# Optimization experiments

Hardware: AMD Instinct MI355X
Metric: run time of the kernel (lower is better)

Reference implementation:

```python
import jax, jax.numpy as jnp
import numpy as np

B, NK, TK, H = 16, 2048, 4096, 256


def setup_inputs() -> dict:
    key = jax.random.key(0)
    ks = jax.random.split(key, 9)
    s = 0.02  # init scale for weights
    return {
        "s_t_hat": jax.random.normal(ks[0], (B, 2 * H), dtype=jnp.float32),
        "encoder_outputs_node": jax.random.normal(ks[1], (B, NK, H), dtype=jnp.float32),
        "node_to_token": jax.random.uniform(ks[2], (B, NK, TK), dtype=jnp.float32),
        "enc_padding_mask_node": jnp.ones((B, NK), dtype=jnp.float32),
        "graph": jax.random.uniform(ks[3], (B, NK, NK), dtype=jnp.float32),
        "flow": jax.random.uniform(ks[4], (B, NK), dtype=jnp.float32),
        "W_c_w": jax.random.normal(ks[5], (1, H), dtype=jnp.float32) * s,
        "enc_proj_w": jax.random.normal(ks[6], (H, H), dtype=jnp.float32) * s,
        "dec_proj_w": jax.random.normal(ks[7], (2 * H, H), dtype=jnp.float32) * s,
        "dec_proj_b": jnp.zeros((H,), dtype=jnp.float32),
        "v_node_w": jax.random.normal(ks[8], (H, 1), dtype=jnp.float32) * s,
    }


def reference(s_t_hat, encoder_outputs_node, node_to_token, enc_padding_mask_node,
              graph, flow, W_c_w, enc_proj_w, dec_proj_w, dec_proj_b, v_node_w):
    # additive attention scoring over graph nodes
    enc_feat = jnp.einsum('bkh,hd->bkd', encoder_outputs_node, enc_proj_w)   # (b,nk,h)
    dec_fea = s_t_hat @ dec_proj_w + dec_proj_b                              # (b,h)
    _flow_feature = flow[..., None] @ W_c_w  # computed in original but unused (dead code)
    e = jnp.tanh(enc_feat + dec_fea[:, None, :])                             # (b,nk,h)
    scores = jnp.squeeze(e @ v_node_w, -1)                                   # (b,nk)
    # masked softmax with renormalization
    attn_ = jax.nn.softmax(scores, axis=1) * enc_padding_mask_node
    attn = attn_ / jnp.sum(attn_, axis=1, keepdims=True)                     # (b,nk)
    # project node attention to token space, renormalize
    tok_ = jnp.einsum('bk,bkt->bt', attn, node_to_token)                     # (b,tk)
    tok = tok_ / jnp.sum(tok_, axis=1, keepdims=True)
    # context vector
    c_t = jnp.einsum('bk,bkh->bh', attn, encoder_outputs_node)               # (b,h)
    # multi-hop graph diffusion
    one_hop = jnp.einsum('bk,bkm->bm', attn, graph)                          # (b,nk)
    two_hop = jnp.einsum('bk,bkm->bm', one_hop, graph)                       # (b,nk)
    flow_out = attn * 0.33333 + one_hop * 0.33333 + two_hop * 0.33333        # (b,nk)
    return (c_t, attn, tok, flow_out)
```

## Files before the change

### kernel.cpp

```cpp
#include <hip/hip_runtime.h>
#include <cstddef>

#define BB 16
#define NK 2048
#define TK 4096
#define HH 256
#define H2 512

__global__ void k_dec_fea(const float* __restrict__ s_t_hat,
                          const float* __restrict__ Wd,
                          const float* __restrict__ bd,
                          float* __restrict__ dec_fea) {
    int b = blockIdx.x, ks = blockIdx.y;
    int d = threadIdx.x;
    __shared__ float s[64];
    if (d < 64) s[d] = s_t_hat[b * H2 + ks * 64 + d];
    __syncthreads();
    float acc = (ks == 0) ? bd[d] : 0.f;
    #pragma unroll
    for (int j = 0; j < 64; ++j)
        acc = fmaf(s[j], Wd[(ks * 64 + j) * HH + d], acc);
    atomicAdd(&dec_fea[b * HH + d], acc);
}

__global__ __launch_bounds__(256) void k_scores(const float* __restrict__ enc,
                         const float* __restrict__ Wenc,
                         const float* __restrict__ dec_fea,
                         const float* __restrict__ v,
                         float* __restrict__ scores) {
    int b   = blockIdx.y;
    int k0  = blockIdx.x * 32;
    int tid = threadIdx.x;
    int lane = tid & 63;
    int wv   = tid >> 6;

    __shared__ float4 encSV[32 * 64];
    const float4* baseV = (const float4*)(enc + ((size_t)b * NK + k0) * HH);
    #pragma unroll
    for (int r = 0; r < 8; ++r) encSV[r * 256 + tid] = baseV[r * 256 + tid];
    __syncthreads();

    const float4* Wv = (const float4*)Wenc;
    float4 acc[8];
    #pragma unroll
    for (int i = 0; i < 8; ++i) acc[i] = make_float4(0.f, 0.f, 0.f, 0.f);

    for (int h4 = 0; h4 < 64; ++h4) {
        float4 w0 = Wv[(h4 * 4 + 0) * 64 + lane];
        float4 w1 = Wv[(h4 * 4 + 1) * 64 + lane];
        float4 w2 = Wv[(h4 * 4 + 2) * 64 + lane];
        float4 w3 = Wv[(h4 * 4 + 3) * 64 + lane];
        #pragma unroll
        for (int i = 0; i < 8; ++i) {
            float4 e = encSV[(wv * 8 + i) * 64 + h4];
            acc[i].x = fmaf(e.x, w0.x, acc[i].x); acc[i].y = fmaf(e.x, w0.y, acc[i].y);
            acc[i].z = fmaf(e.x, w0.z, acc[i].z); acc[i].w = fmaf(e.x, w0.w, acc[i].w);
            acc[i].x = fmaf(e.y, w1.x, acc[i].x); acc[i].y = fmaf(e.y, w1.y, acc[i].y);
            acc[i].z = fmaf(e.y, w1.z, acc[i].z); acc[i].w = fmaf(e.y, w1.w, acc[i].w);
            acc[i].x = fmaf(e.z, w2.x, acc[i].x); acc[i].y = fmaf(e.z, w2.y, acc[i].y);
            acc[i].z = fmaf(e.z, w2.z, acc[i].z); acc[i].w = fmaf(e.z, w2.w, acc[i].w);
            acc[i].x = fmaf(e.w, w3.x, acc[i].x); acc[i].y = fmaf(e.w, w3.y, acc[i].y);
            acc[i].z = fmaf(e.w, w3.z, acc[i].z); acc[i].w = fmaf(e.w, w3.w, acc[i].w);
        }
    }

    float4 df = ((const float4*)(dec_fea + b * HH))[lane];
    float4 vv = ((const float4*)v)[lane];
    #pragma unroll
    for (int i = 0; i < 8; ++i) {
        float p = tanhf(acc[i].x + df.x) * vv.x
                + tanhf(acc[i].y + df.y) * vv.y
                + tanhf(acc[i].z + df.z) * vv.z
                + tanhf(acc[i].w + df.w) * vv.w;
        #pragma unroll
        for (int off = 32; off > 0; off >>= 1) p += __shfl_down(p, off, 64);
        if (lane == 0) scores[b * NK + k0 + wv * 8 + i] = p;
    }
}

__global__ void k_softmax(const float* __restrict__ scores,
                          const float* __restrict__ mask,
                          float* __restrict__ attn) {
    int b = blockIdx.x, tid = threadIdx.x;
    int lane = tid & 63, wv = tid >> 6;
    __shared__ float redmax[4], redsum[4];
    float vals[8];
    float m = -1e30f;
    #pragma unroll
    for (int r = 0; r < 8; ++r) {
        vals[r] = scores[b * NK + r * 256 + tid];
        m = fmaxf(m, vals[r]);
    }
    #pragma unroll
    for (int off = 1; off < 64; off <<= 1) m = fmaxf(m, __shfl_xor(m, off, 64));
    if (lane == 0) redmax[wv] = m;
    __syncthreads();
    m = fmaxf(fmaxf(redmax[0], redmax[1]), fmaxf(redmax[2], redmax[3]));
    float s = 0.f;
    #pragma unroll
    for (int r = 0; r < 8; ++r) {
        float e = __expf(vals[r] - m) * mask[b * NK + r * 256 + tid];
        vals[r] = e;
        s += e;
    }
    #pragma unroll
    for (int off = 1; off < 64; off <<= 1) s += __shfl_xor(s, off, 64);
    if (lane == 0) redsum[wv] = s;
    __syncthreads();
    s = redsum[0] + redsum[1] + redsum[2] + redsum[3];
    float inv = 1.f / s;
    #pragma unroll
    for (int r = 0; r < 8; ++r) attn[b * NK + r * 256 + tid] = vals[r] * inv;
}

__global__ void k_ct(const float* __restrict__ attn,
                     const float* __restrict__ enc,
                     float* __restrict__ out) {
    int b = blockIdx.y;
    int k0 = blockIdx.x * 64;
    int h = threadIdx.x;
    const float* e  = enc + ((size_t)b * NK + k0) * HH;
    const float* wb = attn + b * NK + k0;
    float acc = 0.f;
    #pragma unroll 8
    for (int k = 0; k < 64; ++k) acc = fmaf(wb[k], e[(size_t)k * HH + h], acc);
    atomicAdd(&out[b * HH + h], acc);
}

template <int NCOLS, int KCH>
__global__ __launch_bounds__(256) void k_vecmat(const float* __restrict__ w,
                         const float* __restrict__ M,
                         float* __restrict__ out) {
    constexpr int KR = NK / KCH;
    int b  = blockIdx.z;
    int k0 = blockIdx.y * KR;
    int t  = blockIdx.x * 1024 + threadIdx.x * 4;
    __shared__ float sw[KR];
    for (int i = threadIdx.x; i < KR; i += 256) sw[i] = w[b * NK + k0 + i];
    __syncthreads();
    const float4* Mv = (const float4*)(M + (size_t)b * NK * NCOLS
                                         + (size_t)k0 * NCOLS) + (t >> 2);
    float4 acc = make_float4(0.f, 0.f, 0.f, 0.f);
    #pragma unroll 8
    for (int k = 0; k < KR; ++k) {
        float a = sw[k];
        float4 vv = Mv[(size_t)k * (NCOLS / 4)];
        acc.x = fmaf(a, vv.x, acc.x);
        acc.y = fmaf(a, vv.y, acc.y);
        acc.z = fmaf(a, vv.z, acc.z);
        acc.w = fmaf(a, vv.w, acc.w);
    }
    float* o = out + b * NCOLS + t;
    atomicAdd(o + 0, acc.x);
    atomicAdd(o + 1, acc.y);
    atomicAdd(o + 2, acc.z);
    atomicAdd(o + 3, acc.w);
}

__global__ void k_flowout(const float* __restrict__ attn,
                          const float* __restrict__ oh,
                          const float* __restrict__ th,
                          float* __restrict__ out) {
    int i = blockIdx.x * 256 + threadIdx.x;
    out[i] = (attn[i] + oh[i] + th[i]) * 0.33333f;
}

__global__ void k_toknorm(const float* __restrict__ tok_raw,
                          float* __restrict__ out) {
    int b = blockIdx.x, tid = threadIdx.x;
    int lane = tid & 63, wv = tid >> 6;
    __shared__ float redsum[4];
    float vals[16];
    float s = 0.f;
    #pragma unroll
    for (int r = 0; r < 16; ++r) {
        vals[r] = tok_raw[b * TK + r * 256 + tid];
        s += vals[r];
    }
    #pragma unroll
    for (int off = 1; off < 64; off <<= 1) s += __shfl_xor(s, off, 64);
    if (lane == 0) redsum[wv] = s;
    __syncthreads();
    s = redsum[0] + redsum[1] + redsum[2] + redsum[3];
    float inv = 1.f / s;
    #pragma unroll
    for (int r = 0; r < 16; ++r) out[b * TK + r * 256 + tid] = vals[r] * inv;
}

extern "C" void kernel_launch(void* const* d_in, const int* in_sizes, int n_in,
                              void* d_out, int out_size, void* d_ws, size_t ws_size,
                              hipStream_t stream) {
    const float* s_t_hat = (const float*)d_in[0];
    const float* enc     = (const float*)d_in[1];
    const float* n2t     = (const float*)d_in[2];
    const float* mask    = (const float*)d_in[3];
    const float* graph   = (const float*)d_in[4];
    const float* Wenc    = (const float*)d_in[7];
    const float* Wdec    = (const float*)d_in[8];
    const float* bdec    = (const float*)d_in[9];
    const float* vnode   = (const float*)d_in[10];

    float* out = (float*)d_out;
    float* ws  = (float*)d_ws;

    float* dec_fea = ws;
    float* scores  = ws + 4096;
    float* tok_raw = ws + 36864;
    float* one_hop = ws + 102400;
    float* two_hop = ws + 135168;

    float* c_t   = out;
    float* attn  = out + 4096;
    float* tok   = out + 36864;
    float* flowo = out + 102400;

    hipMemsetAsync(dec_fea, 0, 4096 * sizeof(float), stream);
    hipMemsetAsync(c_t, 0, 4096 * sizeof(float), stream);
    hipMemsetAsync(tok_raw, 0, (65536 + 32768 + 32768) * sizeof(float), stream);

    k_dec_fea<<<dim3(BB, 8), 256, 0, stream>>>(s_t_hat, Wdec, bdec, dec_fea);
    k_scores<<<dim3(NK / 32, BB), 256, 0, stream>>>(enc, Wenc, dec_fea, vnode, scores);
    k_softmax<<<BB, 256, 0, stream>>>(scores, mask, attn);
    k_ct<<<dim3(32, BB), 256, 0, stream>>>(attn, enc, c_t);
    k_vecmat<NK, 32><<<dim3(2, 32, BB), 256, 0, stream>>>(attn, graph, one_hop);
    k_vecmat<NK, 32><<<dim3(2, 32, BB), 256, 0, stream>>>(one_hop, graph, two_hop);
    k_flowout<<<(BB * NK) / 256, 256, 0, stream>>>(attn, one_hop, two_hop, flowo);
    k_vecmat<TK, 16><<<dim3(4, 16, BB), 256, 0, stream>>>(attn, n2t, tok_raw);
    k_toknorm<<<BB, 256, 0, stream>>>(tok_raw, tok);
}
```

Before: 1.006 ms.

## Replace atomic accumulation with partial buffers and separate reductions, reverse second graph pass

After: 1.034 ms. +2.8%, slower.

```diff
diff --git a/kernel.cpp b/kernel.cpp
--- a/kernel.cpp
+++ b/kernel.cpp
@@ -11,16 +11,15 @@
                           const float* __restrict__ Wd,
                           const float* __restrict__ bd,
                           float* __restrict__ dec_fea) {
-    int b = blockIdx.x, ks = blockIdx.y;
-    int d = threadIdx.x;
-    __shared__ float s[64];
-    if (d < 64) s[d] = s_t_hat[b * H2 + ks * 64 + d];
-    __syncthreads();
-    float acc = (ks == 0) ? bd[d] : 0.f;
-    #pragma unroll
-    for (int j = 0; j < 64; ++j)
-        acc = fmaf(s[j], Wd[(ks * 64 + j) * HH + d], acc);
-    atomicAdd(&dec_fea[b * HH + d], acc);
+    int b = blockIdx.x, d = threadIdx.x;
+    __shared__ float s[H2];
+    s[d]       = s_t_hat[b * H2 + d];
+    s[d + HH]  = s_t_hat[b * H2 + HH + d];
+    __syncthreads();
+    float acc = bd[d];
+    #pragma unroll 8
+    for (int j = 0; j < H2; ++j) acc = fmaf(s[j], Wd[j * HH + d], acc);
+    dec_fea[b * HH + d] = acc;
 }
 
 __global__ __launch_bounds__(256) void k_scores(const float* __restrict__ enc,
@@ -115,34 +114,55 @@
 
 __global__ void k_ct(const float* __restrict__ attn,
                      const float* __restrict__ enc,
-                     float* __restrict__ out) {
+                     float* __restrict__ ctp) {
     int b = blockIdx.y;
-    int k0 = blockIdx.x * 64;
+    int kc = blockIdx.x;
     int h = threadIdx.x;
-    const float* e  = enc + ((size_t)b * NK + k0) * HH;
-    const float* wb = attn + b * NK + k0;
+    const float* e  = enc + ((size_t)b * NK + kc * 64) * HH;
+    const float* wb = attn + b * NK + kc * 64;
     float acc = 0.f;
     #pragma unroll 8
     for (int k = 0; k < 64; ++k) acc = fmaf(wb[k], e[(size_t)k * HH + h], acc);
-    atomicAdd(&out[b * HH + h], acc);
-}
-
-template <int NCOLS, int KCH>
-__global__ __launch_bounds__(256) void k_vecmat(const float* __restrict__ w,
+    ctp[((size_t)b * 32 + kc) * HH + h] = acc;
+}
+
+__global__ void k_ct_red(const float* __restrict__ ctp,
+                         float* __restrict__ c_t) {
+    int b = blockIdx.x, h = threadIdx.x;
+    float s = 0.f;
+    #pragma unroll
+    for (int c = 0; c < 32; ++c) s += ctp[((size_t)b * 32 + c) * HH + h];
+    c_t[b * HH + h] = s;
+}
+
+template <int NCOLS, int KCH, int WCH, bool REV>
+__global__ __launch_bounds__(256) void k_vecmat_p(const float* __restrict__ w,
                          const float* __restrict__ M,
-                         float* __restrict__ out) {
+                         float* __restrict__ outp) {
     constexpr int KR = NK / KCH;
     int b  = blockIdx.z;
-    int k0 = blockIdx.y * KR;
+    int ky = blockIdx.y;
+    int k0 = ky * KR;
     int t  = blockIdx.x * 1024 + threadIdx.x * 4;
     __shared__ float sw[KR];
-    for (int i = threadIdx.x; i < KR; i += 256) sw[i] = w[b * NK + k0 + i];
+    if (WCH == 0) {
+        for (int i = threadIdx.x; i < KR; i += 256) sw[i] = w[b * NK + k0 + i];
+    } else {
+        for (int i = threadIdx.x; i < KR; i += 256) {
+            float s = 0.f;
+            #pragma unroll
+            for (int c = 0; c < WCH; ++c)
+                s += w[((size_t)b * WCH + c) * NK + k0 + i];
+            sw[i] = s;
+        }
+    }
     __syncthreads();
     const float4* Mv = (const float4*)(M + (size_t)b * NK * NCOLS
                                          + (size_t)k0 * NCOLS) + (t >> 2);
     float4 acc = make_float4(0.f, 0.f, 0.f, 0.f);
     #pragma unroll 8
-    for (int k = 0; k < KR; ++k) {
+    for (int kk = 0; kk < KR; ++kk) {
+        int k = REV ? (KR - 1 - kk) : kk;
         float a = sw[k];
         float4 vv = Mv[(size_t)k * (NCOLS / 4)];
         acc.x = fmaf(a, vv.x, acc.x);
@@ -150,22 +170,25 @@
         acc.z = fmaf(a, vv.z, acc.z);
         acc.w = fmaf(a, vv.w, acc.w);
     }
-    float* o = out + b * NCOLS + t;
-    atomicAdd(o + 0, acc.x);
-    atomicAdd(o + 1, acc.y);
-    atomicAdd(o + 2, acc.z);
-    atomicAdd(o + 3, acc.w);
+    *(float4*)(outp + ((size_t)b * KCH + ky) * NCOLS + t) = acc;
 }
 
 __global__ void k_flowout(const float* __restrict__ attn,
-                          const float* __restrict__ oh,
-                          const float* __restrict__ th,
+                          const float* __restrict__ ohp,
+                          const float* __restrict__ thp,
                           float* __restrict__ out) {
     int i = blockIdx.x * 256 + threadIdx.x;
-    out[i] = (attn[i] + oh[i] + th[i]) * 0.33333f;
-}
-
-__global__ void k_toknorm(const float* __restrict__ tok_raw,
+    int b = i >> 11, k = i & (NK - 1);
+    float oh = 0.f, th = 0.f;
+    #pragma unroll
+    for (int c = 0; c < 32; ++c) {
+        oh += ohp[((size_t)b * 32 + c) * NK + k];
+        th += thp[((size_t)b * 32 + c) * NK + k];
+    }
+    out[i] = (attn[i] + oh + th) * 0.33333f;
+}
+
+__global__ void k_toknorm(const float* __restrict__ tokp,
                           float* __restrict__ out) {
     int b = blockIdx.x, tid = threadIdx.x;
     int lane = tid & 63, wv = tid >> 6;
@@ -174,8 +197,12 @@
     float s = 0.f;
     #pragma unroll
     for (int r = 0; r < 16; ++r) {
-        vals[r] = tok_raw[b * TK + r * 256 + tid];
-        s += vals[r];
+        int col = r * 256 + tid;
+        float v = 0.f;
+        #pragma unroll
+        for (int c = 0; c < 16; ++c) v += tokp[((size_t)b * 16 + c) * TK + col];
+        vals[r] = v;
+        s += v;
     }
     #pragma unroll
     for (int off = 1; off < 64; off <<= 1) s += __shfl_xor(s, off, 64);
@@ -205,26 +232,24 @@
 
     float* dec_fea = ws;
     float* scores  = ws + 4096;
-    float* tok_raw = ws + 36864;
-    float* one_hop = ws + 102400;
-    float* two_hop = ws + 135168;
+    float* ctp     = ws + 36864;
+    float* ohp     = ws + 167936;
+    float* thp     = ws + 1216512;
+    float* tokp    = ws + 2265088;
 
     float* c_t   = out;
     float* attn  = out + 4096;
     float* tok   = out + 36864;
     float* flowo = out + 102400;
 
-    hipMemsetAsync(dec_fea, 0, 4096 * sizeof(float), stream);
-    hipMemsetAsync(c_t, 0, 4096 * sizeof(float), stream);
-    hipMemsetAsync(tok_raw, 0, (65536 + 32768 + 32768) * sizeof(float), stream);
-
-    k_dec_fea<<<dim3(BB, 8), 256, 0, stream>>>(s_t_hat, Wdec, bdec, dec_fea);
+    k_dec_fea<<<BB, 256, 0, stream>>>(s_t_hat, Wdec, bdec, dec_fea);
     k_scores<<<dim3(NK / 32, BB), 256, 0, stream>>>(enc, Wenc, dec_fea, vnode, scores);
     k_softmax<<<BB, 256, 0, stream>>>(scores, mask, attn);
-    k_ct<<<dim3(32, BB), 256, 0, stream>>>(attn, enc, c_t);
-    k_vecmat<NK, 32><<<dim3(2, 32, BB), 256, 0, stream>>>(attn, graph, one_hop);
-    k_vecmat<NK, 32><<<dim3(2, 32, BB), 256, 0, stream>>>(one_hop, graph, two_hop);
-    k_flowout<<<(BB * NK) / 256, 256, 0, stream>>>(attn, one_hop, two_hop, flowo);
-    k_vecmat<TK, 16><<<dim3(4, 16, BB), 256, 0, stream>>>(attn, n2t, tok_raw);
-    k_toknorm<<<BB, 256, 0, stream>>>(tok_raw, tok);
-}
+    k_ct<<<dim3(32, BB), 256, 0, stream>>>(attn, enc, ctp);
+    k_ct_red<<<BB, 256, 0, stream>>>(ctp, c_t);
+    k_vecmat_p<NK, 32, 0,  false><<<dim3(2, 32, BB), 256, 0, stream>>>(attn, graph, ohp);
+    k_vecmat_p<NK, 32, 32, true ><<<dim3(2, 32, BB), 256, 0, stream>>>(ohp,  graph, thp);
+    k_flowout<<<(BB * NK) / 256, 256, 0, stream>>>(attn, ohp, thp, flowo);
+    k_vecmat_p<TK, 16, 0,  false><<<dim3(4, 16, BB), 256, 0, stream>>>(attn, n2t, tokp);
+    k_toknorm<<<BB, 256, 0, stream>>>(tokp, tok);
+}
```
